# Kernel tuning notes

Measured on AMD Instinct MI355X. Metric: run time of the kernel, lower is better.

Reference implementation:

```python
import jax, jax.numpy as jnp
import numpy as np

B, L, CIN, DLOI, NPTS0, NPTS1, H = 2, 5000, 256, 128, 32, 8, 256
HALF = DLOI // 2
EPS = 1e-5


def _bn_params(k, c):
    k1, k2, k3, k4 = jax.random.split(k, 4)
    gamma = 1.0 + 0.1 * jax.random.normal(k1, (c,), jnp.float32)
    beta = 0.1 * jax.random.normal(k2, (c,), jnp.float32)
    mean = 0.1 * jax.random.normal(k3, (c,), jnp.float32)
    var = 0.5 + jax.random.uniform(k4, (c,), jnp.float32)
    return jnp.stack([gamma, beta, mean, var])  # [4, c]


def setup_inputs():
    key = jax.random.key(0)
    ks = jax.random.split(key, 12)
    feature = jax.random.normal(ks[0], (B, CIN, H, H), jnp.float32)
    lines = jax.random.uniform(ks[1], (B, L, 2, 2), jnp.float32, minval=0.0, maxval=255.0)
    w_fc1 = 0.05 * jax.random.normal(ks[2], (DLOI, CIN), jnp.float32)
    b_fc1 = jnp.zeros((DLOI,), jnp.float32)
    bn1 = _bn_params(ks[3], DLOI)
    c1_w = 0.1 * jax.random.normal(ks[4], (HALF, DLOI), jnp.float32)
    c1_b = jnp.zeros((HALF,), jnp.float32)
    bn2 = _bn_params(ks[5], HALF)
    c2_w = 0.1 * jax.random.normal(ks[6], (HALF, HALF, 3), jnp.float32)
    c2_b = jnp.zeros((HALF,), jnp.float32)
    bn3 = _bn_params(ks[7], HALF)
    c3_w = 0.1 * jax.random.normal(ks[8], (DLOI, HALF), jnp.float32)
    c3_b = jnp.zeros((DLOI,), jnp.float32)
    w_fc2 = 0.03 * jax.random.normal(ks[9], (4, DLOI * NPTS1), jnp.float32)
    b_fc2 = jnp.zeros((4,), jnp.float32)
    return {"feature": feature, "lines": lines, "w_fc1": w_fc1, "b_fc1": b_fc1,
            "bn1": bn1, "c1_w": c1_w, "c1_b": c1_b, "bn2": bn2, "c2_w": c2_w,
            "c2_b": c2_b, "bn3": bn3, "c3_w": c3_w, "c3_b": c3_b,
            "w_fc2": w_fc2, "b_fc2": b_fc2}


def _bn(v, p):
    # v: [N, C, P], p: [4, C] = gamma, beta, running_mean, running_var (eval mode)
    scale = (p[0] * jax.lax.rsqrt(p[3] + EPS))[None, :, None]
    shift = p[1][None, :, None]
    return (v - p[2][None, :, None]) * scale + shift


def _forward(feature, lines, w_fc1, b_fc1, bn1, c1_w, c1_b, bn2, c2_w, c2_b,
             bn3, c3_w, c3_b, w_fc2, b_fc2):
    # fc1: 1x1 conv over backbone feature -> [B, DLOI, H, H]
    x = jnp.einsum('bchw,oc->bohw', feature, w_fc1) + b_fc1[None, :, None, None]

    # sample NPTS0 points along each line: p = p0*lam + p1*(1-lam) - 0.5
    lam = jnp.linspace(0.0, 1.0, NPTS0, dtype=jnp.float32)[:, None]  # [NPTS0, 1]
    p = lines[:, :, 0:1, :] * lam + lines[:, :, 1:2, :] * (1.0 - lam) - 0.5  # [B,L,NPTS0,2]
    px, py = p[..., 0], p[..., 1]
    px0 = jnp.clip(jnp.floor(px), 0.0, H - 1.0)
    py0 = jnp.clip(jnp.floor(py), 0.0, H - 1.0)
    px1 = jnp.clip(px0 + 1.0, 0.0, H - 1.0)
    py1 = jnp.clip(py0 + 1.0, 0.0, H - 1.0)
    i0, j0 = px0.astype(jnp.int32), py0.astype(jnp.int32)
    i1, j1 = px1.astype(jnp.int32), py1.astype(jnp.int32)
    w00 = (px1 - px) * (py1 - py)
    w10 = (px - px0) * (py1 - py)
    w01 = (px1 - px) * (py - py0)
    w11 = (px - px0) * (py - py0)

    def gather_one(feat, i0b, j0b, i1b, j1b, a, b, c, d):
        # feat [C,H,W]; indices/weights [L, NPTS0] -> [C, L, NPTS0]
        return (feat[:, i0b, j0b] * a + feat[:, i1b, j0b] * b
                + feat[:, i0b, j1b] * c + feat[:, i1b, j1b] * d)

    xp = jax.vmap(gather_one)(x, i0, j0, i1, j1, w00, w10, w01, w11)  # [B,C,L,NPTS0]
    xp = xp.transpose(0, 2, 1, 3).reshape(B * L, DLOI, NPTS0)

    # MaxPool1d(kernel=4, stride=4): NPTS0 -> NPTS1
    xp = xp.reshape(B * L, DLOI, NPTS1, NPTS0 // NPTS1).max(-1)

    # Bottleneck1D (eval-mode BN): x + op(x)
    h = jax.nn.relu(_bn(xp, bn1))
    h = jnp.einsum('ncp,oc->nop', h, c1_w) + c1_b[None, :, None]
    h = jax.nn.relu(_bn(h, bn2))
    h = jax.lax.conv_general_dilated(h, c2_w, window_strides=(1,), padding=((1, 1),),
                                     dimension_numbers=('NCH', 'OIH', 'NCH')) + c2_b[None, :, None]
    h = jax.nn.relu(_bn(h, bn3))
    h = jnp.einsum('ncp,oc->nop', h, c3_w) + c3_b[None, :, None]
    y = xp + h

    # fc2: ReLU + Linear(DLOI*NPTS1 -> 4), then softmax scores
    flat = y.reshape(B * L, DLOI * NPTS1)
    logits = jax.nn.relu(flat) @ w_fc2.T + b_fc2
    s = jax.nn.softmax(logits, axis=-1)
    return s


def reference(feature, lines, w_fc1, b_fc1, bn1, c1_w, c1_b, bn2, c2_w, c2_b,
              bn3, c3_w, c3_b, w_fc2, b_fc2):
    return _forward(feature, lines, w_fc1, b_fc1, bn1, c1_w, c1_b, bn2, c2_w,
                    c2_b, bn3, c3_w, c3_b, w_fc2, b_fc2)
```

## Files before the change

kernel.cpp:

```cpp
#include <hip/hip_runtime.h>
#include <math.h>
#include <stdint.h>

#define HH 256
#define HW 65536
#define CIN 256
#define DLOI 128
#define NLINES 10000
#define LPB 5000

typedef _Float16 h2v  __attribute__((ext_vector_type(2)));
typedef _Float16 f16x8 __attribute__((ext_vector_type(8)));
typedef float    f32x4 __attribute__((ext_vector_type(4)));

__device__ __forceinline__ h2v u2h(unsigned int u) { return __builtin_bit_cast(h2v, u); }
__device__ __forceinline__ unsigned int h2u(h2v h) { return __builtin_bit_cast(unsigned int, h); }

__device__ __forceinline__ float fdot2(h2v a, unsigned int w, float c) {
#if __has_builtin(__builtin_amdgcn_fdot2)
    return __builtin_amdgcn_fdot2(a, u2h(w), c, false);
#else
    h2v b = u2h(w);
    return c + (float)a[0] * (float)b[0] + (float)a[1] * (float)b[1];
#endif
}

__device__ __forceinline__ h2v relu2(h2v a) {
    h2v z = (h2v)(_Float16)0.f;
#if __has_builtin(__builtin_elementwise_max)
    return __builtin_elementwise_max(a, z);
#else
    h2v r; r[0] = a[0] > z[0] ? a[0] : z[0]; r[1] = a[1] > z[1] ? a[1] : z[1]; return r;
#endif
}
__device__ __forceinline__ h2v hmax2v(h2v a, h2v b) {
#if __has_builtin(__builtin_elementwise_max)
    return __builtin_elementwise_max(a, b);
#else
    h2v r; r[0] = a[0] > b[0] ? a[0] : b[0]; r[1] = a[1] > b[1] ? a[1] : b[1]; return r;
#endif
}

__global__ __launch_bounds__(256) void prep_small(
    const float* __restrict__ w_fc1, const float* __restrict__ c1w,
    const float* __restrict__ c2w,  const float* __restrict__ c3w,
    const float* __restrict__ wfc2, const float* __restrict__ bn1,
    const float* __restrict__ bn2,  const float* __restrict__ bn3,
    _Float16* __restrict__ wf16, unsigned int* __restrict__ c1w16,
    unsigned int* __restrict__ c2w16, unsigned int* __restrict__ c3w16,
    unsigned int* __restrict__ wfc2p, unsigned int* __restrict__ bn_pk)
{
    int i = blockIdx.x * 256 + threadIdx.x;
    if (i < 32768) { wf16[i] = (_Float16)w_fc1[i]; return; }
    i -= 32768;
    if (i < 4096) {
        int c2 = i >> 6, o = i & 63;
        h2v v = { (_Float16)c1w[o * 128 + 2 * c2], (_Float16)c1w[o * 128 + 2 * c2 + 1] };
        c1w16[c2 * 64 + o] = h2u(v); return;
    }
    i -= 4096;
    if (i < 6144) {
        int o = i & 63, rem = i >> 6; int tap = rem % 3, i2 = rem / 3;
        h2v v = { (_Float16)c2w[(o * 64 + 2 * i2) * 3 + tap],
                  (_Float16)c2w[(o * 64 + 2 * i2 + 1) * 3 + tap] };
        c2w16[(i2 * 3 + tap) * 64 + o] = h2u(v); return;
    }
    i -= 6144;
    if (i < 4096) {
        int o = i & 127, i2 = i >> 7;
        h2v v = { (_Float16)c3w[o * 64 + 2 * i2], (_Float16)c3w[o * 64 + 2 * i2 + 1] };
        c3w16[i2 * 128 + o] = h2u(v); return;
    }
    i -= 4096;
    if (i < 2048) {
        int c2 = i & 63, p = (i >> 6) & 7, j = i >> 9;
        h2v v = { (_Float16)wfc2[j * 1024 + (2 * c2) * 8 + p],
                  (_Float16)wfc2[j * 1024 + (2 * c2 + 1) * 8 + p] };
        wfc2p[(j * 8 + p) * 64 + c2] = h2u(v); return;
    }
    i -= 2048;
    if (i < 128) {
        const float* bn; int C, base, hcount;
        if (i < 64)      { bn = bn1; C = 128; base = 0;   hcount = 64; }
        else if (i < 96) { bn = bn2; C = 64;  base = 128; hcount = 32; i -= 64; }
        else             { bn = bn3; C = 64;  base = 192; hcount = 32; i -= 96; }
        int c0 = 2 * i, c1 = 2 * i + 1;
        float s0 = bn[c0] * rsqrtf(bn[3 * C + c0] + 1e-5f);
        float s1 = bn[c1] * rsqrtf(bn[3 * C + c1] + 1e-5f);
        float h0 = bn[C + c0] - bn[2 * C + c0] * s0;
        float h1 = bn[C + c1] - bn[2 * C + c1] * s1;
        h2v sv = { (_Float16)s0, (_Float16)s1 };
        h2v hv = { (_Float16)h0, (_Float16)h1 };
        bn_pk[base + i] = h2u(sv);
        bn_pk[base + hcount + i] = h2u(hv);
    }
}

__global__ __launch_bounds__(256, 4) void fc1_fused(
    const float* __restrict__ feat,
    const _Float16* __restrict__ W,
    const float* __restrict__ bias,
    unsigned int* __restrict__ X)
{
    __shared__ float Tf[32 * 132];
    __shared__ _Float16 Wl[128 * 40];
    const int t = threadIdx.x;
    const int lane = t & 63, wave = t >> 6;
    const int wm = wave & 1, wn = wave >> 1;
    const int pix0g = blockIdx.x << 7;
    const int b = blockIdx.x >> 9;
    const int pix0l = pix0g & 65535;
    const float* fbase = feat + (size_t)b * (256u * 65536u) + pix0l;

    f32x4 acc[4][4];
#pragma unroll
    for (int a = 0; a < 4; a++)
#pragma unroll
        for (int c = 0; c < 4; c++) acc[a][c] = (f32x4)0.f;

    for (int ks = 0; ks < 8; ks++) {
        const int k0 = ks * 32;
        __syncthreads();
#pragma unroll
        for (int r = 0; r < 4; r++) {
            int idx = t + r * 256;
            int c = idx >> 5, p4 = idx & 31;
            float4 v = *(const float4*)(fbase + (size_t)(k0 + c) * 65536 + p4 * 4);
            *(float4*)&Tf[c * 132 + p4 * 4] = v;
        }
#pragma unroll
        for (int r = 0; r < 2; r++) {
            int idx = t + r * 256;
            int row = idx >> 2, ko = (idx & 3) * 8;
            *(uint4*)&Wl[row * 40 + ko] = *(const uint4*)(W + row * 256 + k0 + ko);
        }
        __syncthreads();
        f16x8 af[4], bf[4];
#pragma unroll
        for (int mt = 0; mt < 4; mt++)
            af[mt] = *(const f16x8*)&Wl[(wm * 64 + mt * 16 + (lane & 15)) * 40 + (lane >> 4) * 8];
#pragma unroll
        for (int nt = 0; nt < 4; nt++) {
            int q = wn * 64 + nt * 16 + (lane & 15);
            int cb = (lane >> 4) * 8;
            f16x8 v;
#pragma unroll
            for (int j = 0; j < 8; j++) v[j] = (_Float16)Tf[(cb + j) * 132 + q];
            bf[nt] = v;
        }
#pragma unroll
        for (int mt = 0; mt < 4; mt++)
#pragma unroll
            for (int nt = 0; nt < 4; nt++)
                acc[mt][nt] = __builtin_amdgcn_mfma_f32_16x16x32_f16(af[mt], bf[nt], acc[mt][nt], 0, 0, 0);
    }
#pragma unroll
    for (int mt = 0; mt < 4; mt++) {
        int o = wm * 64 + mt * 16 + (lane >> 4) * 4;
        float4 b4 = *(const float4*)(bias + o);
#pragma unroll
        for (int nt = 0; nt < 4; nt++) {
            int pix = pix0g + wn * 64 + nt * 16 + (lane & 15);
            f32x4 a = acc[mt][nt];
            h2v lo = { (_Float16)(a[0] + b4.x), (_Float16)(a[1] + b4.y) };
            h2v hi = { (_Float16)(a[2] + b4.z), (_Float16)(a[3] + b4.w) };
            uint2 v = { h2u(lo), h2u(hi) };
            *(uint2*)(X + (size_t)pix * 64 + (o >> 1)) = v;
        }
    }
}

__global__ __launch_bounds__(256, 4) void line_v3(
    const unsigned int* __restrict__ X,
    const float* __restrict__ lines,
    const unsigned int* __restrict__ c1w16, const float* __restrict__ c1b,
    const unsigned int* __restrict__ c2w16, const float* __restrict__ c2b,
    const unsigned int* __restrict__ c3w16, const float* __restrict__ c3b,
    const unsigned int* __restrict__ wfc2p, const float* __restrict__ bfc2,
    const unsigned int* __restrict__ bn_pk,
    float* __restrict__ out)
{
    __shared__ int geoB[256];
    __shared__ unsigned int geoWA[256], geoWB[256];
    __shared__ h2v xp[64 * 65];
    __shared__ h2v hb[32 * 65];
    __shared__ h2v ap[32 * 73];
    __shared__ float red[128];

    const int t = threadIdx.x;
    const int n0 = blockIdx.x * 8;
    const int col = t & 63;
    const int og = t >> 6;

    {
        int l = t >> 5, k = t & 31;
        int n = n0 + l;
        float4 ln = *(const float4*)(lines + n * 4);
        float lam = (float)k / 31.0f;
        float px = ln.x * lam + ln.z * (1.f - lam) - 0.5f;
        float py = ln.y * lam + ln.w * (1.f - lam) - 0.5f;
        float px0 = fminf(fmaxf(floorf(px), 0.f), 255.f);
        float py0 = fminf(fmaxf(floorf(py), 0.f), 255.f);
        float dx = px - px0, dy = py - py0;
        float ex = 1.f - dx, ey = 1.f - dy;
        h2v wA = { (_Float16)(ex * ey), (_Float16)(dx * ey) };
        h2v wB = { (_Float16)(ex * dy), (_Float16)(dx * dy) };
        int b = (n >= LPB) ? 1 : 0;
        int pixflat = (b << 16) + ((int)px0 << 8) + (int)py0;
        geoB[t] = pixflat << 6;
        geoWA[t] = h2u(wA); geoWB[t] = h2u(wB);
    }
    __syncthreads();

    {
        const int c8 = t & 15;
        const int sub = t >> 4;
        const int line = sub >> 1;
        const int gbase = (sub & 1) * 4;
        const uint4* xq = (const uint4*)X;
#pragma unroll
        for (int lg = 0; lg < 4; lg++) {
            int g = gbase + lg;
            int ptb = line * 32 + g * 4;
            h2v m0, m1, m2, m3;
#pragma unroll
            for (int s = 0; s < 4; s++) {
                int pt = ptb + s;
                int base4 = (geoB[pt] >> 2) + c8;
                h2v wA = u2h(geoWA[pt]), wB = u2h(geoWB[pt]);
                uint4 q00 = xq[base4];
                uint4 q10 = xq[base4 + 4096];
                uint4 q01 = xq[base4 + 16];
                uint4 q11 = xq[base4 + 4112];
                h2v w00 = { wA[0], wA[0] }, w10 = { wA[1], wA[1] };
                h2v w01 = { wB[0], wB[0] }, w11 = { wB[1], wB[1] };
                h2v v0 = u2h(q00.x) * w00 + u2h(q10.x) * w10 + u2h(q01.x) * w01 + u2h(q11.x) * w11;
                h2v v1 = u2h(q00.y) * w00 + u2h(q10.y) * w10 + u2h(q01.y) * w01 + u2h(q11.y) * w11;
                h2v v2 = u2h(q00.z) * w00 + u2h(q10.z) * w10 + u2h(q01.z) * w01 + u2h(q11.z) * w11;
                h2v v3 = u2h(q00.w) * w00 + u2h(q10.w) * w10 + u2h(q01.w) * w01 + u2h(q11.w) * w11;
                if (s == 0) { m0 = v0; m1 = v1; m2 = v2; m3 = v3; }
                else { m0 = hmax2v(m0, v0); m1 = hmax2v(m1, v1);
                       m2 = hmax2v(m2, v2); m3 = hmax2v(m3, v3); }
            }
            int colw = line * 8 + g;
            xp[(c8 * 4 + 0) * 65 + colw] = m0;
            xp[(c8 * 4 + 1) * 65 + colw] = m1;
            xp[(c8 * 4 + 2) * 65 + colw] = m2;
            xp[(c8 * 4 + 3) * 65 + colw] = m3;
        }
    }
    __syncthreads();

    {
        const int obU = __builtin_amdgcn_readfirstlane(og * 16);
        float acc[16];
#pragma unroll
        for (int i = 0; i < 16; i++) acc[i] = c1b[obU + i];
#pragma unroll 8
        for (int c2 = 0; c2 < 64; c2++) {
            h2v sc = u2h(bn_pk[c2]), sh = u2h(bn_pk[64 + c2]);
            h2v av = relu2(xp[c2 * 65 + col] * sc + sh);
            unsigned int wv[16];
#pragma unroll
            for (int q = 0; q < 4; q++)
                *(uint4*)&wv[q * 4] = *(const uint4*)(c1w16 + c2 * 64 + obU + q * 4);
#pragma unroll
            for (int i = 0; i < 16; i++) acc[i] = fdot2(av, wv[i], acc[i]);
        }
#pragma unroll
        for (int j = 0; j < 8; j++) {
            h2v v = { (_Float16)acc[2 * j], (_Float16)acc[2 * j + 1] };
            hb[(obU / 2 + j) * 65 + col] = v;
        }
    }
    __syncthreads();

    {
        int c2 = t >> 3, l = t & 7;
        h2v sc = u2h(bn_pk[128 + c2]), sh = u2h(bn_pk[160 + c2]);
        h2v z = (h2v)(_Float16)0.f;
        ap[c2 * 73 + l * 9] = z;
#pragma unroll
        for (int p = 0; p < 8; p++)
            ap[c2 * 73 + l * 9 + 1 + p] = relu2(hb[c2 * 65 + l * 8 + p] * sc + sh);
        if (l == 7) ap[c2 * 73 + 72] = z;
    }
    __syncthreads();

    {
        const int obU = __builtin_amdgcn_readfirstlane(og * 16);
        const int l = col >> 3, p = col & 7;
        const int pos0 = l * 9 + p;
        float acc[16];
#pragma unroll
        for (int i = 0; i < 16; i++) acc[i] = c2b[obU + i];
#pragma unroll 2
        for (int i2 = 0; i2 < 32; i2++) {
            h2v a0 = ap[i2 * 73 + pos0];
            h2v a1 = ap[i2 * 73 + pos0 + 1];
            h2v a2 = ap[i2 * 73 + pos0 + 2];
            unsigned int wv[48];
#pragma unroll
            for (int tap = 0; tap < 3; tap++)
#pragma unroll
                for (int q = 0; q < 4; q++)
                    *(uint4*)&wv[tap * 16 + q * 4] =
                        *(const uint4*)(c2w16 + (i2 * 3 + tap) * 64 + obU + q * 4);
#pragma unroll
            for (int i = 0; i < 16; i++) {
                acc[i] = fdot2(a0, wv[i], acc[i]);
                acc[i] = fdot2(a1, wv[16 + i], acc[i]);
                acc[i] = fdot2(a2, wv[32 + i], acc[i]);
            }
        }
#pragma unroll
        for (int j = 0; j < 8; j++) {
            h2v v = { (_Float16)acc[2 * j], (_Float16)acc[2 * j + 1] };
            hb[(obU / 2 + j) * 65 + col] = v;
        }
    }
    __syncthreads();

#pragma unroll
    for (int r = 0; r < 8; r++) {
        int idx = t + 256 * r;
        int c2 = idx >> 6, cl = idx & 63;
        h2v sc = u2h(bn_pk[192 + c2]), sh = u2h(bn_pk[224 + c2]);
        ap[c2 * 64 + cl] = relu2(hb[c2 * 65 + cl] * sc + sh);
    }
    __syncthreads();

    {
        const int obU = __builtin_amdgcn_readfirstlane(og * 32);
        float acc[32];
#pragma unroll
        for (int i = 0; i < 32; i++) acc[i] = c3b[obU + i];
#pragma unroll 2
        for (int i2 = 0; i2 < 32; i2++) {
            h2v av = ap[i2 * 64 + col];
            unsigned int wv[32];
#pragma unroll
            for (int q = 0; q < 8; q++)
                *(uint4*)&wv[q * 4] = *(const uint4*)(c3w16 + i2 * 128 + obU + q * 4);
#pragma unroll
            for (int i = 0; i < 32; i++) acc[i] = fdot2(av, wv[i], acc[i]);
        }
        const int p = col & 7, l = col >> 3;
        h2v yv[16];
#pragma unroll
        for (int j = 0; j < 16; j++) {
            h2v hv = { (_Float16)acc[2 * j], (_Float16)acc[2 * j + 1] };
            yv[j] = relu2(xp[(obU / 2 + j) * 65 + col] + hv);
        }
        float aj[4] = { 0.f, 0.f, 0.f, 0.f };
#pragma unroll
        for (int j = 0; j < 4; j++) {
            unsigned int wv2[16];
#pragma unroll
            for (int q = 0; q < 4; q++)
                *(uint4*)&wv2[q * 4] = *(const uint4*)(wfc2p + (j * 8 + p) * 64 + obU / 2 + q * 4);
#pragma unroll
            for (int j16 = 0; j16 < 16; j16++) aj[j] = fdot2(yv[j16], wv2[j16], aj[j]);
        }
#pragma unroll
        for (int off = 4; off > 0; off >>= 1) {
#pragma unroll
            for (int j = 0; j < 4; j++) aj[j] += __shfl_down(aj[j], off, 8);
        }
        if ((t & 7) == 0) {
#pragma unroll
            for (int j = 0; j < 4; j++) red[og * 32 + l * 4 + j] = aj[j];
        }
    }
    __syncthreads();

    if (t < 8) {
        float lg[4];
#pragma unroll
        for (int j = 0; j < 4; j++)
            lg[j] = bfc2[j] + red[t * 4 + j] + red[32 + t * 4 + j]
                  + red[64 + t * 4 + j] + red[96 + t * 4 + j];
        float mx = fmaxf(fmaxf(lg[0], lg[1]), fmaxf(lg[2], lg[3]));
        float e0 = expf(lg[0] - mx), e1 = expf(lg[1] - mx);
        float e2 = expf(lg[2] - mx), e3 = expf(lg[3] - mx);
        float s = 1.f / (e0 + e1 + e2 + e3);
        float4 r = { e0 * s, e1 * s, e2 * s, e3 * s };
        *(float4*)(out + (size_t)(n0 + t) * 4) = r;
    }
}

extern "C" void kernel_launch(void* const* d_in, const int* in_sizes, int n_in,
                              void* d_out, int out_size, void* d_ws, size_t ws_size,
                              hipStream_t stream) {
    const float* feature = (const float*)d_in[0];
    const float* lines   = (const float*)d_in[1];
    const float* w_fc1   = (const float*)d_in[2];
    const float* b_fc1   = (const float*)d_in[3];
    const float* bn1     = (const float*)d_in[4];
    const float* c1_w    = (const float*)d_in[5];
    const float* c1_b    = (const float*)d_in[6];
    const float* bn2     = (const float*)d_in[7];
    const float* c2_w    = (const float*)d_in[8];
    const float* c2_b    = (const float*)d_in[9];
    const float* bn3     = (const float*)d_in[10];
    const float* c3_w    = (const float*)d_in[11];
    const float* c3_b    = (const float*)d_in[12];
    const float* w_fc2   = (const float*)d_in[13];
    const float* b_fc2   = (const float*)d_in[14];
    float* out = (float*)d_out;

    char* ws = (char*)d_ws;
    unsigned int* X     = (unsigned int*)ws;
    _Float16*     wf16  = (_Float16*)(ws + 33554432);
    unsigned int* c1w16 = (unsigned int*)(ws + 33619968);
    unsigned int* c2w16 = (unsigned int*)(ws + 33636352);
    unsigned int* c3w16 = (unsigned int*)(ws + 33660928);
    unsigned int* wfc2p = (unsigned int*)(ws + 33677312);
    unsigned int* bn_pk = (unsigned int*)(ws + 33685504);

    prep_small<<<193, 256, 0, stream>>>(w_fc1, c1_w, c2_w, c3_w, w_fc2, bn1, bn2, bn3,
                                        wf16, c1w16, c2w16, c3w16, wfc2p, bn_pk);
    fc1_fused<<<1024, 256, 0, stream>>>(feature, wf16, b_fc1, X);
    line_v3<<<1250, 256, 0, stream>>>(X, lines, c1w16, c1_b, c2w16, c2_b,
                                      c3w16, c3_b, wfc2p, b_fc2, bn_pk, out);
}
```

Baseline: 313.7 us.

## Pre-pack fc1 weights into MFMA fragments, double-buffer features, persistent line kernel

The fc1 kernel now reads A-operand weights directly from global memory, pre-swizzled into MFMA fragment order by the prep kernel, so the weight LDS stage is gone. Feature loads are prefetched one k-step ahead into registers and written as packed fp16 into a double-buffered LDS tile, leaving one barrier per iteration. The line kernel becomes persistent: 1024 blocks pull line groups from an atomic counter. This trades some extra register pressure and an atomic per group for hiding load latency and removing per-block launch overhead and tail imbalance.

```diff
diff --git a/kernel.cpp b/kernel.cpp
--- a/kernel.cpp
+++ b/kernel.cpp
@@ -8,6 +8,7 @@
 #define DLOI 128
 #define NLINES 10000
 #define LPB 5000
+#define NGROUPS 1250
 
 typedef _Float16 h2v  __attribute__((ext_vector_type(2)));
 typedef _Float16 f16x8 __attribute__((ext_vector_type(8)));
@@ -15,6 +16,9 @@
 
 __device__ __forceinline__ h2v u2h(unsigned int u) { return __builtin_bit_cast(h2v, u); }
 __device__ __forceinline__ unsigned int h2u(h2v h) { return __builtin_bit_cast(unsigned int, h); }
+__device__ __forceinline__ unsigned int pk2u(float a, float b) {
+    return __builtin_bit_cast(unsigned int, __builtin_amdgcn_cvt_pkrtz(a, b));
+}
 
 __device__ __forceinline__ float fdot2(h2v a, unsigned int w, float c) {
 #if __has_builtin(__builtin_amdgcn_fdot2)
@@ -46,13 +50,28 @@
     const float* __restrict__ c2w,  const float* __restrict__ c3w,
     const float* __restrict__ wfc2, const float* __restrict__ bn1,
     const float* __restrict__ bn2,  const float* __restrict__ bn3,
-    _Float16* __restrict__ wf16, unsigned int* __restrict__ c1w16,
+    uint4* __restrict__ Wf4, unsigned int* __restrict__ c1w16,
     unsigned int* __restrict__ c2w16, unsigned int* __restrict__ c3w16,
-    unsigned int* __restrict__ wfc2p, unsigned int* __restrict__ bn_pk)
+    unsigned int* __restrict__ wfc2p, unsigned int* __restrict__ bn_pk,
+    unsigned int* __restrict__ cnt)
 {
+    if (blockIdx.x == 0 && threadIdx.x == 0) *cnt = 0;
     int i = blockIdx.x * 256 + threadIdx.x;
-    if (i < 32768) { wf16[i] = (_Float16)w_fc1[i]; return; }
-    i -= 32768;
+    if (i < 4096) {
+        int lane = i & 63, mt = (i >> 6) & 3, wm = (i >> 8) & 1, ks = i >> 9;
+        int row = wm * 64 + mt * 16 + (lane & 15);
+        int kb = ks * 32 + (lane >> 4) * 8;
+        const float* src = w_fc1 + row * 256 + kb;
+        unsigned int q[4];
+#pragma unroll
+        for (int j2 = 0; j2 < 4; j2++) {
+            h2v v = { (_Float16)src[2 * j2], (_Float16)src[2 * j2 + 1] };
+            q[j2] = h2u(v);
+        }
+        uint4 o = { q[0], q[1], q[2], q[3] };
+        Wf4[i] = o; return;
+    }
+    i -= 4096;
     if (i < 4096) {
         int c2 = i >> 6, o = i & 63;
         h2v v = { (_Float16)c1w[o * 128 + 2 * c2], (_Float16)c1w[o * 128 + 2 * c2 + 1] };
@@ -96,21 +115,26 @@
     }
 }
 
-__global__ __launch_bounds__(256, 4) void fc1_fused(
+__global__ __launch_bounds__(256, 4) void fc1_v3(
     const float* __restrict__ feat,
-    const _Float16* __restrict__ W,
+    const uint4* __restrict__ Wf4,
     const float* __restrict__ bias,
     unsigned int* __restrict__ X)
 {
-    __shared__ float Tf[32 * 132];
-    __shared__ _Float16 Wl[128 * 40];
+    __shared__ unsigned int Fl[2][128 * 20];
     const int t = threadIdx.x;
     const int lane = t & 63, wave = t >> 6;
     const int wm = wave & 1, wn = wave >> 1;
     const int pix0g = blockIdx.x << 7;
     const int b = blockIdx.x >> 9;
-    const int pix0l = pix0g & 65535;
-    const float* fbase = feat + (size_t)b * (256u * 65536u) + pix0l;
+    const float* fbase = feat + (size_t)b * (256u * 65536u) + (pix0g & 65535);
+    const int cp = t & 15, pg = t >> 4;
+    const float* f0 = fbase + (size_t)(2 * cp) * HW + pg * 8;
+    const float* f1 = fbase + (size_t)(2 * cp + 1) * HW + pg * 8;
+
+    float4 a0, a1, b0, b1;
+    a0 = *(const float4*)(f0);     a1 = *(const float4*)(f0 + 4);
+    b0 = *(const float4*)(f1);     b1 = *(const float4*)(f1 + 4);
 
     f32x4 acc[4][4];
 #pragma unroll
@@ -118,42 +142,44 @@
 #pragma unroll
         for (int c = 0; c < 4; c++) acc[a][c] = (f32x4)0.f;
 
+    auto stage = [&](int buf) {
+        unsigned int* w = &Fl[buf][(pg * 8) * 20 + cp];
+        w[0]   = pk2u(a0.x, b0.x);
+        w[20]  = pk2u(a0.y, b0.y);
+        w[40]  = pk2u(a0.z, b0.z);
+        w[60]  = pk2u(a0.w, b0.w);
+        w[80]  = pk2u(a1.x, b1.x);
+        w[100] = pk2u(a1.y, b1.y);
+        w[120] = pk2u(a1.z, b1.z);
+        w[140] = pk2u(a1.w, b1.w);
+    };
+    stage(0);
+
     for (int ks = 0; ks < 8; ks++) {
-        const int k0 = ks * 32;
-        __syncthreads();
-#pragma unroll
-        for (int r = 0; r < 4; r++) {
-            int idx = t + r * 256;
-            int c = idx >> 5, p4 = idx & 31;
-            float4 v = *(const float4*)(fbase + (size_t)(k0 + c) * 65536 + p4 * 4);
-            *(float4*)&Tf[c * 132 + p4 * 4] = v;
-        }
-#pragma unroll
-        for (int r = 0; r < 2; r++) {
-            int idx = t + r * 256;
-            int row = idx >> 2, ko = (idx & 3) * 8;
-            *(uint4*)&Wl[row * 40 + ko] = *(const uint4*)(W + row * 256 + k0 + ko);
-        }
-        __syncthreads();
-        f16x8 af[4], bf[4];
+        uint4 afu[4];
 #pragma unroll
         for (int mt = 0; mt < 4; mt++)
-            af[mt] = *(const f16x8*)&Wl[(wm * 64 + mt * 16 + (lane & 15)) * 40 + (lane >> 4) * 8];
+            afu[mt] = Wf4[ks * 512 + wm * 256 + mt * 64 + lane];
+        if (ks < 7) {
+            const float* g0 = f0 + (size_t)(ks + 1) * 32 * HW;
+            const float* g1 = f1 + (size_t)(ks + 1) * 32 * HW;
+            a0 = *(const float4*)(g0);     a1 = *(const float4*)(g0 + 4);
+            b0 = *(const float4*)(g1);     b1 = *(const float4*)(g1 + 4);
+        }
+        __syncthreads();
+        const unsigned int* Fb = Fl[ks & 1];
 #pragma unroll
         for (int nt = 0; nt < 4; nt++) {
-            int q = wn * 64 + nt * 16 + (lane & 15);
-            int cb = (lane >> 4) * 8;
-            f16x8 v;
-#pragma unroll
-            for (int j = 0; j < 8; j++) v[j] = (_Float16)Tf[(cb + j) * 132 + q];
-            bf[nt] = v;
-        }
-#pragma unroll
-        for (int mt = 0; mt < 4; mt++)
-#pragma unroll
-            for (int nt = 0; nt < 4; nt++)
-                acc[mt][nt] = __builtin_amdgcn_mfma_f32_16x16x32_f16(af[mt], bf[nt], acc[mt][nt], 0, 0, 0);
-    }
+            int pix = wn * 64 + nt * 16 + (lane & 15);
+            f16x8 bf = *(const f16x8*)&Fb[pix * 20 + (lane >> 4) * 4];
+#pragma unroll
+            for (int mt = 0; mt < 4; mt++)
+                acc[mt][nt] = __builtin_amdgcn_mfma_f32_16x16x32_f16(
+                    __builtin_bit_cast(f16x8, afu[mt]), bf, acc[mt][nt], 0, 0, 0);
+        }
+        if (ks < 7) stage((ks + 1) & 1);
+    }
+
 #pragma unroll
     for (int mt = 0; mt < 4; mt++) {
         int o = wm * 64 + mt * 16 + (lane >> 4) * 4;
@@ -170,14 +196,14 @@
     }
 }
 
-__global__ __launch_bounds__(256, 4) void line_v3(
+__global__ __launch_bounds__(256, 4) void line_v4(
     const unsigned int* __restrict__ X,
     const float* __restrict__ lines,
     const unsigned int* __restrict__ c1w16, const float* __restrict__ c1b,
     const unsigned int* __restrict__ c2w16, const float* __restrict__ c2b,
     const unsigned int* __restrict__ c3w16, const float* __restrict__ c3b,
     const unsigned int* __restrict__ wfc2p, const float* __restrict__ bfc2,
-    const unsigned int* __restrict__ bn_pk,
+    const unsigned int* __restrict__ bn_pk, unsigned int* __restrict__ cnt,
     float* __restrict__ out)
 {
     __shared__ int geoB[256];
@@ -186,206 +212,215 @@
     __shared__ h2v hb[32 * 65];
     __shared__ h2v ap[32 * 73];
     __shared__ float red[128];
+    __shared__ int s_g;
 
     const int t = threadIdx.x;
-    const int n0 = blockIdx.x * 8;
     const int col = t & 63;
     const int og = t >> 6;
 
-    {
-        int l = t >> 5, k = t & 31;
-        int n = n0 + l;
-        float4 ln = *(const float4*)(lines + n * 4);
-        float lam = (float)k / 31.0f;
-        float px = ln.x * lam + ln.z * (1.f - lam) - 0.5f;
-        float py = ln.y * lam + ln.w * (1.f - lam) - 0.5f;
-        float px0 = fminf(fmaxf(floorf(px), 0.f), 255.f);
-        float py0 = fminf(fmaxf(floorf(py), 0.f), 255.f);
-        float dx = px - px0, dy = py - py0;
-        float ex = 1.f - dx, ey = 1.f - dy;
-        h2v wA = { (_Float16)(ex * ey), (_Float16)(dx * ey) };
-        h2v wB = { (_Float16)(ex * dy), (_Float16)(dx * dy) };
-        int b = (n >= LPB) ? 1 : 0;
-        int pixflat = (b << 16) + ((int)px0 << 8) + (int)py0;
-        geoB[t] = pixflat << 6;
-        geoWA[t] = h2u(wA); geoWB[t] = h2u(wB);
-    }
-    __syncthreads();
-
-    {
-        const int c8 = t & 15;
-        const int sub = t >> 4;
-        const int line = sub >> 1;
-        const int gbase = (sub & 1) * 4;
-        const uint4* xq = (const uint4*)X;
-#pragma unroll
-        for (int lg = 0; lg < 4; lg++) {
-            int g = gbase + lg;
-            int ptb = line * 32 + g * 4;
-            h2v m0, m1, m2, m3;
-#pragma unroll
-            for (int s = 0; s < 4; s++) {
-                int pt = ptb + s;
-                int base4 = (geoB[pt] >> 2) + c8;
-                h2v wA = u2h(geoWA[pt]), wB = u2h(geoWB[pt]);
-                uint4 q00 = xq[base4];
-                uint4 q10 = xq[base4 + 4096];
-                uint4 q01 = xq[base4 + 16];
-                uint4 q11 = xq[base4 + 4112];
-                h2v w00 = { wA[0], wA[0] }, w10 = { wA[1], wA[1] };
-                h2v w01 = { wB[0], wB[0] }, w11 = { wB[1], wB[1] };
-                h2v v0 = u2h(q00.x) * w00 + u2h(q10.x) * w10 + u2h(q01.x) * w01 + u2h(q11.x) * w11;
-                h2v v1 = u2h(q00.y) * w00 + u2h(q10.y) * w10 + u2h(q01.y) * w01 + u2h(q11.y) * w11;
-                h2v v2 = u2h(q00.z) * w00 + u2h(q10.z) * w10 + u2h(q01.z) * w01 + u2h(q11.z) * w11;
-                h2v v3 = u2h(q00.w) * w00 + u2h(q10.w) * w10 + u2h(q01.w) * w01 + u2h(q11.w) * w11;
-                if (s == 0) { m0 = v0; m1 = v1; m2 = v2; m3 = v3; }
-                else { m0 = hmax2v(m0, v0); m1 = hmax2v(m1, v1);
-                       m2 = hmax2v(m2, v2); m3 = hmax2v(m3, v3); }
-            }
-            int colw = line * 8 + g;
-            xp[(c8 * 4 + 0) * 65 + colw] = m0;
-            xp[(c8 * 4 + 1) * 65 + colw] = m1;
-            xp[(c8 * 4 + 2) * 65 + colw] = m2;
-            xp[(c8 * 4 + 3) * 65 + colw] = m3;
-        }
-    }
-    __syncthreads();
-
-    {
-        const int obU = __builtin_amdgcn_readfirstlane(og * 16);
-        float acc[16];
-#pragma unroll
-        for (int i = 0; i < 16; i++) acc[i] = c1b[obU + i];
+    for (;;) {
+        if (t == 0) s_g = (int)atomicAdd(cnt, 1u);
+        __syncthreads();
+        const int g = s_g;
+        if (g >= NGROUPS) break;
+        const int n0 = g * 8;
+
+        {
+            int l = t >> 5, k = t & 31;
+            int n = n0 + l;
+            float4 ln = *(const float4*)(lines + n * 4);
+            float lam = (float)k / 31.0f;
+            float px = ln.x * lam + ln.z * (1.f - lam) - 0.5f;
+            float py = ln.y * lam + ln.w * (1.f - lam) - 0.5f;
+            float px0 = fminf(fmaxf(floorf(px), 0.f), 255.f);
+            float py0 = fminf(fmaxf(floorf(py), 0.f), 255.f);
+            float dx = px - px0, dy = py - py0;
+            float ex = 1.f - dx, ey = 1.f - dy;
+            h2v wA = { (_Float16)(ex * ey), (_Float16)(dx * ey) };
+            h2v wB = { (_Float16)(ex * dy), (_Float16)(dx * dy) };
+            int b = (n >= LPB) ? 1 : 0;
+            int pixflat = (b << 16) + ((int)px0 << 8) + (int)py0;
+            geoB[t] = pixflat << 6;
+            geoWA[t] = h2u(wA); geoWB[t] = h2u(wB);
+        }
+        __syncthreads();
+
+        {
+            const int c8 = t & 15;
+            const int sub = t >> 4;
+            const int line = sub >> 1;
+            const int gbase = (sub & 1) * 4;
+            const uint4* xq = (const uint4*)X;
+#pragma unroll
+            for (int lg = 0; lg < 4; lg++) {
+                int gi = gbase + lg;
+                int ptb = line * 32 + gi * 4;
+                h2v m0, m1, m2, m3;
+#pragma unroll
+                for (int s = 0; s < 4; s++) {
+                    int pt = ptb + s;
+                    int base4 = (geoB[pt] >> 2) + c8;
+                    h2v wA = u2h(geoWA[pt]), wB = u2h(geoWB[pt]);
+                    uint4 q00 = xq[base4];
+                    uint4 q10 = xq[base4 + 4096];
+                    uint4 q01 = xq[base4 + 16];
+                    uint4 q11 = xq[base4 + 4112];
+                    h2v w00 = { wA[0], wA[0] }, w10 = { wA[1], wA[1] };
+                    h2v w01 = { wB[0], wB[0] }, w11 = { wB[1], wB[1] };
+                    h2v v0 = u2h(q00.x) * w00 + u2h(q10.x) * w10 + u2h(q01.x) * w01 + u2h(q11.x) * w11;
+                    h2v v1 = u2h(q00.y) * w00 + u2h(q10.y) * w10 + u2h(q01.y) * w01 + u2h(q11.y) * w11;
+                    h2v v2 = u2h(q00.z) * w00 + u2h(q10.z) * w10 + u2h(q01.z) * w01 + u2h(q11.z) * w11;
+                    h2v v3 = u2h(q00.w) * w00 + u2h(q10.w) * w10 + u2h(q01.w) * w01 + u2h(q11.w) * w11;
+                    if (s == 0) { m0 = v0; m1 = v1; m2 = v2; m3 = v3; }
+                    else { m0 = hmax2v(m0, v0); m1 = hmax2v(m1, v1);
+                           m2 = hmax2v(m2, v2); m3 = hmax2v(m3, v3); }
+                }
+                int colw = line * 8 + gi;
+                xp[(c8 * 4 + 0) * 65 + colw] = m0;
+                xp[(c8 * 4 + 1) * 65 + colw] = m1;
+                xp[(c8 * 4 + 2) * 65 + colw] = m2;
+                xp[(c8 * 4 + 3) * 65 + colw] = m3;
+            }
+        }
+        __syncthreads();
+
+        {
+            const int obU = __builtin_amdgcn_readfirstlane(og * 16);
+            float acc[16];
+#pragma unroll
+            for (int i = 0; i < 16; i++) acc[i] = c1b[obU + i];
 #pragma unroll 8
-        for (int c2 = 0; c2 < 64; c2++) {
-            h2v sc = u2h(bn_pk[c2]), sh = u2h(bn_pk[64 + c2]);
-            h2v av = relu2(xp[c2 * 65 + col] * sc + sh);
-            unsigned int wv[16];
-#pragma unroll
-            for (int q = 0; q < 4; q++)
-                *(uint4*)&wv[q * 4] = *(const uint4*)(c1w16 + c2 * 64 + obU + q * 4);
-#pragma unroll
-            for (int i = 0; i < 16; i++) acc[i] = fdot2(av, wv[i], acc[i]);
-        }
-#pragma unroll
-        for (int j = 0; j < 8; j++) {
-            h2v v = { (_Float16)acc[2 * j], (_Float16)acc[2 * j + 1] };
-            hb[(obU / 2 + j) * 65 + col] = v;
-        }
-    }
-    __syncthreads();
-
-    {
-        int c2 = t >> 3, l = t & 7;
-        h2v sc = u2h(bn_pk[128 + c2]), sh = u2h(bn_pk[160 + c2]);
-        h2v z = (h2v)(_Float16)0.f;
-        ap[c2 * 73 + l * 9] = z;
-#pragma unroll
-        for (int p = 0; p < 8; p++)
-            ap[c2 * 73 + l * 9 + 1 + p] = relu2(hb[c2 * 65 + l * 8 + p] * sc + sh);
-        if (l == 7) ap[c2 * 73 + 72] = z;
-    }
-    __syncthreads();
-
-    {
-        const int obU = __builtin_amdgcn_readfirstlane(og * 16);
-        const int l = col >> 3, p = col & 7;
-        const int pos0 = l * 9 + p;
-        float acc[16];
-#pragma unroll
-        for (int i = 0; i < 16; i++) acc[i] = c2b[obU + i];
+            for (int c2 = 0; c2 < 64; c2++) {
+                h2v sc = u2h(bn_pk[c2]), sh = u2h(bn_pk[64 + c2]);
+                h2v av = relu2(xp[c2 * 65 + col] * sc + sh);
+                unsigned int wv[16];
+#pragma unroll
+                for (int q = 0; q < 4; q++)
+                    *(uint4*)&wv[q * 4] = *(const uint4*)(c1w16 + c2 * 64 + obU + q * 4);
+#pragma unroll
+                for (int i = 0; i < 16; i++) acc[i] = fdot2(av, wv[i], acc[i]);
+            }
+#pragma unroll
+            for (int j = 0; j < 8; j++) {
+                h2v v = { (_Float16)acc[2 * j], (_Float16)acc[2 * j + 1] };
+                hb[(obU / 2 + j) * 65 + col] = v;
+            }
+        }
+        __syncthreads();
+
+        {
+            int c2 = t >> 3, l = t & 7;
+            h2v sc = u2h(bn_pk[128 + c2]), sh = u2h(bn_pk[160 + c2]);
+            h2v z = (h2v)(_Float16)0.f;
+            ap[c2 * 73 + l * 9] = z;
+#pragma unroll
+            for (int p = 0; p < 8; p++)
+                ap[c2 * 73 + l * 9 + 1 + p] = relu2(hb[c2 * 65 + l * 8 + p] * sc + sh);
+            if (l == 7) ap[c2 * 73 + 72] = z;
+        }
+        __syncthreads();
+
+        {
+            const int obU = __builtin_amdgcn_readfirstlane(og * 16);
+            const int l = col >> 3, p = col & 7;
+            const int pos0 = l * 9 + p;
+            float acc[16];
+#pragma unroll
+            for (int i = 0; i < 16; i++) acc[i] = c2b[obU + i];
 #pragma unroll 2
-        for (int i2 = 0; i2 < 32; i2++) {
-            h2v a0 = ap[i2 * 73 + pos0];
-            h2v a1 = ap[i2 * 73 + pos0 + 1];
-            h2v a2 = ap[i2 * 73 + pos0 + 2];
-            unsigned int wv[48];
-#pragma unroll
-            for (int tap = 0; tap < 3; tap++)
+            for (int i2 = 0; i2 < 32; i2++) {
+                h2v aa0 = ap[i2 * 73 + pos0];
+                h2v aa1 = ap[i2 * 73 + pos0 + 1];
+                h2v aa2 = ap[i2 * 73 + pos0 + 2];
+                unsigned int wv[48];
+#pragma unroll
+                for (int tap = 0; tap < 3; tap++)
+#pragma unroll
+                    for (int q = 0; q < 4; q++)
+                        *(uint4*)&wv[tap * 16 + q * 4] =
+                            *(const uint4*)(c2w16 + (i2 * 3 + tap) * 64 + obU + q * 4);
+#pragma unroll
+                for (int i = 0; i < 16; i++) {
+                    acc[i] = fdot2(aa0, wv[i], acc[i]);
+                    acc[i] = fdot2(aa1, wv[16 + i], acc[i]);
+                    acc[i] = fdot2(aa2, wv[32 + i], acc[i]);
+                }
+            }
+#pragma unroll
+            for (int j = 0; j < 8; j++) {
+                h2v v = { (_Float16)acc[2 * j], (_Float16)acc[2 * j + 1] };
+                hb[(obU / 2 + j) * 65 + col] = v;
+            }
+        }
+        __syncthreads();
+
+#pragma unroll
+        for (int r = 0; r < 8; r++) {
+            int idx = t + 256 * r;
+            int c2 = idx >> 6, cl = idx & 63;
+            h2v sc = u2h(bn_pk[192 + c2]), sh = u2h(bn_pk[224 + c2]);
+            ap[c2 * 64 + cl] = relu2(hb[c2 * 65 + cl] * sc + sh);
+        }
+        __syncthreads();
+
+        {
+            const int obU = __builtin_amdgcn_readfirstlane(og * 32);
+            float acc[32];
+#pragma unroll
+            for (int i = 0; i < 32; i++) acc[i] = c3b[obU + i];
+#pragma unroll 2
+            for (int i2 = 0; i2 < 32; i2++) {
+                h2v av = ap[i2 * 64 + col];
+                unsigned int wv[32];
+#pragma unroll
+                for (int q = 0; q < 8; q++)
+                    *(uint4*)&wv[q * 4] = *(const uint4*)(c3w16 + i2 * 128 + obU + q * 4);
+#pragma unroll
+                for (int i = 0; i < 32; i++) acc[i] = fdot2(av, wv[i], acc[i]);
+            }
+            const int p = col & 7, l = col >> 3;
+            h2v yv[16];
+#pragma unroll
+            for (int j = 0; j < 16; j++) {
+                h2v hv = { (_Float16)acc[2 * j], (_Float16)acc[2 * j + 1] };
+                yv[j] = relu2(xp[(obU / 2 + j) * 65 + col] + hv);
+            }
+            float aj[4] = { 0.f, 0.f, 0.f, 0.f };
+#pragma unroll
+            for (int j = 0; j < 4; j++) {
+                unsigned int wv2[16];
 #pragma unroll
                 for (int q = 0; q < 4; q++)
-                    *(uint4*)&wv[tap * 16 + q * 4] =
-                        *(const uint4*)(c2w16 + (i2 * 3 + tap) * 64 + obU + q * 4);
-#pragma unroll
-            for (int i = 0; i < 16; i++) {
-                acc[i] = fdot2(a0, wv[i], acc[i]);
-                acc[i] = fdot2(a1, wv[16 + i], acc[i]);
-                acc[i] = fdot2(a2, wv[32 + i], acc[i]);
-            }
-        }
-#pragma unroll
-        for (int j = 0; j < 8; j++) {
-            h2v v = { (_Float16)acc[2 * j], (_Float16)acc[2 * j + 1] };
-            hb[(obU / 2 + j) * 65 + col] = v;
-        }
-    }
-    __syncthreads();
-
-#pragma unroll
-    for (int r = 0; r < 8; r++) {
-        int idx = t + 256 * r;
-        int c2 = idx >> 6, cl = idx & 63;
-        h2v sc = u2h(bn_pk[192 + c2]), sh = u2h(bn_pk[224 + c2]);
-        ap[c2 * 64 + cl] = relu2(hb[c2 * 65 + cl] * sc + sh);
-    }
-    __syncthreads();
-
-    {
-        const int obU = __builtin_amdgcn_readfirstlane(og * 32);
-        float acc[32];
-#pragma unroll
-        for (int i = 0; i < 32; i++) acc[i] = c3b[obU + i];
-#pragma unroll 2
-        for (int i2 = 0; i2 < 32; i2++) {
-            h2v av = ap[i2 * 64 + col];
-            unsigned int wv[32];
-#pragma unroll
-            for (int q = 0; q < 8; q++)
-                *(uint4*)&wv[q * 4] = *(const uint4*)(c3w16 + i2 * 128 + obU + q * 4);
-#pragma unroll
-            for (int i = 0; i < 32; i++) acc[i] = fdot2(av, wv[i], acc[i]);
-        }
-        const int p = col & 7, l = col >> 3;
-        h2v yv[16];
-#pragma unroll
-        for (int j = 0; j < 16; j++) {
-            h2v hv = { (_Float16)acc[2 * j], (_Float16)acc[2 * j + 1] };
-            yv[j] = relu2(xp[(obU / 2 + j) * 65 + col] + hv);
-        }
-        float aj[4] = { 0.f, 0.f, 0.f, 0.f };
-#pragma unroll
-        for (int j = 0; j < 4; j++) {
-            unsigned int wv2[16];
-#pragma unroll
-            for (int q = 0; q < 4; q++)
-                *(uint4*)&wv2[q * 4] = *(const uint4*)(wfc2p + (j * 8 + p) * 64 + obU / 2 + q * 4);
-#pragma unroll
-            for (int j16 = 0; j16 < 16; j16++) aj[j] = fdot2(yv[j16], wv2[j16], aj[j]);
-        }
-#pragma unroll
-        for (int off = 4; off > 0; off >>= 1) {
-#pragma unroll
-            for (int j = 0; j < 4; j++) aj[j] += __shfl_down(aj[j], off, 8);
-        }
-        if ((t & 7) == 0) {
-#pragma unroll
-            for (int j = 0; j < 4; j++) red[og * 32 + l * 4 + j] = aj[j];
-        }
-    }
-    __syncthreads();
-
-    if (t < 8) {
-        float lg[4];
-#pragma unroll
-        for (int j = 0; j < 4; j++)
-            lg[j] = bfc2[j] + red[t * 4 + j] + red[32 + t * 4 + j]
-                  + red[64 + t * 4 + j] + red[96 + t * 4 + j];
-        float mx = fmaxf(fmaxf(lg[0], lg[1]), fmaxf(lg[2], lg[3]));
-        float e0 = expf(lg[0] - mx), e1 = expf(lg[1] - mx);
-        float e2 = expf(lg[2] - mx), e3 = expf(lg[3] - mx);
-        float s = 1.f / (e0 + e1 + e2 + e3);
-        float4 r = { e0 * s, e1 * s, e2 * s, e3 * s };
-        *(float4*)(out + (size_t)(n0 + t) * 4) = r;
+                    *(uint4*)&wv2[q * 4] = *(const uint4*)(wfc2p + (j * 8 + p) * 64 + obU / 2 + q * 4);
+#pragma unroll
+                for (int j16 = 0; j16 < 16; j16++) aj[j] = fdot2(yv[j16], wv2[j16], aj[j]);
+            }
+#pragma unroll
+            for (int off = 4; off > 0; off >>= 1) {
+#pragma unroll
+                for (int j = 0; j < 4; j++) aj[j] += __shfl_down(aj[j], off, 8);
+            }
+            if ((t & 7) == 0) {
+#pragma unroll
+                for (int j = 0; j < 4; j++) red[og * 32 + l * 4 + j] = aj[j];
+            }
+        }
+        __syncthreads();
+
+        if (t < 8) {
+            float lg[4];
+#pragma unroll
+            for (int j = 0; j < 4; j++)
+                lg[j] = bfc2[j] + red[t * 4 + j] + red[32 + t * 4 + j]
+                      + red[64 + t * 4 + j] + red[96 + t * 4 + j];
+            float mx = fmaxf(fmaxf(lg[0], lg[1]), fmaxf(lg[2], lg[3]));
+            float e0 = expf(lg[0] - mx), e1 = expf(lg[1] - mx);
+            float e2 = expf(lg[2] - mx), e3 = expf(lg[3] - mx);
+            float s = 1.f / (e0 + e1 + e2 + e3);
+            float4 r = { e0 * s, e1 * s, e2 * s, e3 * s };
+            *(float4*)(out + (size_t)(n0 + t) * 4) = r;
+        }
+        __syncthreads();
     }
 }
 
@@ -411,16 +446,17 @@
 
     char* ws = (char*)d_ws;
     unsigned int* X     = (unsigned int*)ws;
-    _Float16*     wf16  = (_Float16*)(ws + 33554432);
+    uint4*        Wf4   = (uint4*)(ws + 33554432);
     unsigned int* c1w16 = (unsigned int*)(ws + 33619968);
     unsigned int* c2w16 = (unsigned int*)(ws + 33636352);
     unsigned int* c3w16 = (unsigned int*)(ws + 33660928);
     unsigned int* wfc2p = (unsigned int*)(ws + 33677312);
     unsigned int* bn_pk = (unsigned int*)(ws + 33685504);
-
-    prep_small<<<193, 256, 0, stream>>>(w_fc1, c1_w, c2_w, c3_w, w_fc2, bn1, bn2, bn3,
-                                        wf16, c1w16, c2w16, c3w16, wfc2p, bn_pk);
-    fc1_fused<<<1024, 256, 0, stream>>>(feature, wf16, b_fc1, X);
-    line_v3<<<1250, 256, 0, stream>>>(X, lines, c1w16, c1_b, c2w16, c2_b,
-                                      c3w16, c3_b, wfc2p, b_fc2, bn_pk, out);
-}
+    unsigned int* cnt   = (unsigned int*)(ws + 33686528);
+
+    prep_small<<<81, 256, 0, stream>>>(w_fc1, c1_w, c2_w, c3_w, w_fc2, bn1, bn2, bn3,
+                                       Wf4, c1w16, c2w16, c3w16, wfc2p, bn_pk, cnt);
+    fc1_v3<<<1024, 256, 0, stream>>>(feature, Wf4, b_fc1, X);
+    line_v4<<<1024, 256, 0, stream>>>(X, lines, c1w16, c1_b, c2w16, c2_b,
+                                      c3w16, c3_b, wfc2p, b_fc2, bn_pk, cnt, out);
+}
```

Result: slower. 357.3 us (+13.9%).
